# Performance work log

Hardware: AMD Instinct MI355X
Metric: run time of the kernel (lower is better)

## Reference

```python
import math
import jax, jax.numpy as jnp
import numpy as np

B, S, D, H = 2, 2048, 1024, 16


def setup_inputs() -> dict:
    key = jax.random.key(0)
    ks = jax.random.split(key, 8)
    scale = 1.0 / math.sqrt(D)
    kv_mask = jax.random.randint(ks[1], (B, S), 0, 2).astype(bool)
    kv_mask = kv_mask.at[:, 0].set(True)  # ensure at least one valid kv per batch
    return {
        "q": jax.random.normal(ks[0], (B, S, D), dtype=jnp.float32),
        "kv_mask": kv_mask,
        "Wq": jax.random.normal(ks[2], (D, D), dtype=jnp.float32) * scale,
        "Wk": jax.random.normal(ks[3], (D, D), dtype=jnp.float32) * scale,
        "Wv": jax.random.normal(ks[4], (D, D), dtype=jnp.float32) * scale,
        "Wo": jax.random.normal(ks[5], (D, D), dtype=jnp.float32) * scale,
        "bo": jax.random.normal(ks[6], (D,), dtype=jnp.float32) * 0.01,
        "num_heads": H,
    }


def _pass_with_mask(x, W, mask, b=None):
    # Linear applied everywhere, output zeroed where mask is False (pass_with_mask)
    y = x @ W.T
    if b is not None:
        y = y + b
    return jnp.where(mask[..., None], y, 0.0)


def reference(q, kv_mask, Wq, Wk, Wv, Wo, bo, num_heads):
    b, s, d = q.shape
    hd = d // num_heads
    q_mask = jnp.ones((b, s), dtype=bool)  # default q_mask in the module
    # self-attention: k = v = q
    qh = _pass_with_mask(q, Wq, q_mask).reshape(b, s, num_heads, hd)
    kh = _pass_with_mask(q, Wk, kv_mask).reshape(b, s, num_heads, hd)
    vh = _pass_with_mask(q, Wv, kv_mask).reshape(b, s, num_heads, hd)
    # scores: note the module scales by sqrt(model_dim), NOT sqrt(head_dim)
    scores = jnp.einsum("bqhd,bkhd->bhqk", qh, kh) / math.sqrt(d)
    mask = (q_mask[:, :, None] & kv_mask[:, None, :])[:, None, :, :]  # [b,1,q,k]
    scores = jnp.where(mask, scores, -jnp.inf)
    attn = jax.nn.softmax(scores, axis=-1)
    attn = jnp.where(mask, attn, 0.0)
    out = jnp.einsum("bhqk,bkhd->bqhd", attn, vh).reshape(b, s, d)
    return _pass_with_mask(out, Wo, q_mask, bo)
```

## Files before the change

### kernel.cpp

```cpp
#include <hip/hip_runtime.h>
#include <math.h>

#define B_ 2
#define S_ 2048
#define DM 1024
#define NH 16
#define HD 64

typedef unsigned short u16;
typedef unsigned int u32;
typedef __attribute__((ext_vector_type(8))) short bf16x8;
typedef __attribute__((ext_vector_type(4))) float f32x4;

#define C2SCALE 0.0450842200277800f

__device__ __forceinline__ u16 f2bf(float x) {
  unsigned u = __float_as_uint(x);
  u = (u + 0x7FFFu + ((u >> 16) & 1u)) >> 16;
  return (u16)u;
}

__device__ __forceinline__ u32 cvtpk(float lo, float hi) {
  u32 r;
  asm("v_cvt_pk_bf16_f32 %0, %1, %2" : "=v"(r) : "v"(lo), "v"(hi));
  return r;
}

__device__ __forceinline__ float exp2a(float x) {
  float r;
  asm("v_exp_f32 %0, %1" : "=v"(r) : "v"(x));
  return r;
}

__device__ __forceinline__ void gload_lds16(const u16* g, u16* l) {
  __builtin_amdgcn_global_load_lds((const __attribute__((address_space(1))) void*)g,
                                   (__attribute__((address_space(3))) void*)l, 16, 0, 0);
}

__device__ __forceinline__ int sigpos(int w6) {
  return ((w6 >> 5) << 5) | (((w6 >> 2) & 3) << 3) | (((w6 >> 4) & 1) << 2) | (w6 & 3);
}

__global__ void cvt_all(const float* __restrict__ q, const float* __restrict__ Wq,
                        const float* __restrict__ Wk, const float* __restrict__ Wv,
                        const float* __restrict__ Wo, const int* __restrict__ kvm,
                        u16* __restrict__ Xbf, u16* __restrict__ Wcat,
                        u16* __restrict__ Wobf, u16* __restrict__ mwg) {
  const int NQ4 = (B_ * S_ * DM) / 4;
  const int NW4 = (DM * DM) / 4;
  const int total = NQ4 + 4 * NW4;
  int i = blockIdx.x * blockDim.x + threadIdx.x;
  int stride = gridDim.x * blockDim.x;
  for (int t = i; t < B_ * S_; t += stride) {
    int kv = t & (S_ - 1);
    mwg[(t & ~(S_ - 1)) + (kv & ~63) + sigpos(kv & 63)] = kvm[t] ? 0xFFFFu : 0u;
  }
  for (; i < total; i += stride) {
    const float* src;
    u16* dst;
    if (i < NQ4) {
      src = q + (size_t)i * 4; dst = Xbf + (size_t)i * 4;
    } else {
      int t = i - NQ4;
      if (t < NW4)            { src = Wq + (size_t)t * 4; dst = Wcat + (size_t)t * 4; }
      else if (t < 2 * NW4)   { src = Wk + (size_t)(t - NW4) * 4;     dst = Wcat + DM * DM + (size_t)(t - NW4) * 4; }
      else if (t < 3 * NW4)   { src = Wv + (size_t)(t - 2 * NW4) * 4; dst = Wcat + 2 * DM * DM + (size_t)(t - 2 * NW4) * 4; }
      else                    { src = Wo + (size_t)(t - 3 * NW4) * 4; dst = Wobf + (size_t)(t - 3 * NW4) * 4; }
    }
    float4 v = *(const float4*)src;
    ushort4 o;
    o.x = f2bf(v.x); o.y = f2bf(v.y); o.z = f2bf(v.z); o.w = f2bf(v.w);
    *(ushort4*)dst = o;
  }
}

__global__ __launch_bounds__(256, 2) void gemm_bt(
    const u16* __restrict__ A, const u16* __restrict__ Bw, int K,
    u16* __restrict__ qo, u16* __restrict__ ko, u16* __restrict__ vo) {
  __shared__ __align__(16) u16 As[128 * 32];
  __shared__ __align__(16) u16 Bs[128 * 32];
  const int tid = threadIdx.x;
  const int wv = tid >> 6, lane = tid & 63;
  const int g = lane >> 4, c = lane & 15;
  const int wr = wv >> 1, wc = wv & 1;
  const int L = blockIdx.y * gridDim.x + blockIdx.x;
  const int cpx = (gridDim.x * gridDim.y) >> 3;
  const int Ls = (L & 7) * cpx + (L >> 3);
  const int Mb = (Ls & 31) << 7, Nb = (Ls >> 5) << 7;

  f32x4 acc[4][4];
#pragma unroll
  for (int i = 0; i < 4; i++)
#pragma unroll
    for (int j = 0; j < 4; j++) acc[i][j] = f32x4{0.f, 0.f, 0.f, 0.f};

  for (int kb = 0; kb < K; kb += 32) {
#pragma unroll
    for (int it = 0; it < 2; ++it) {
      int id = it * 256 + tid;
      int m = id >> 2, kk = (id & 3) * 8;
      gload_lds16(A + (size_t)(Mb + m) * K + kb + kk, As + (it * 4 + wv) * 512);
      gload_lds16(Bw + (size_t)(Nb + m) * K + kb + kk, Bs + (it * 4 + wv) * 512);
    }
    __syncthreads();
    bf16x8 af[4], bfr[4];
#pragma unroll
    for (int mi = 0; mi < 4; mi++)
      af[mi] = *(const bf16x8*)(As + (wr * 64 + mi * 16 + c) * 32 + g * 8);
#pragma unroll
    for (int ni = 0; ni < 4; ni++)
      bfr[ni] = *(const bf16x8*)(Bs + (wc * 64 + ni * 16 + c) * 32 + g * 8);
#pragma unroll
    for (int mi = 0; mi < 4; mi++)
#pragma unroll
      for (int ni = 0; ni < 4; ni++)
        acc[mi][ni] = __builtin_amdgcn_mfma_f32_16x16x32_bf16(af[mi], bfr[ni], acc[mi][ni], 0, 0, 0);
    __syncthreads();
  }

#pragma unroll
  for (int mi = 0; mi < 4; mi++) {
#pragma unroll
    for (int ni = 0; ni < 4; ni++) {
      int n = Nb + wc * 64 + ni * 16 + c;
      int which = n >> 10, nn = n & 1023;
      int h = nn >> 6, d = nn & 63;
      int row0 = Mb + wr * 64 + mi * 16 + g * 4;
      int b0 = row0 >> 11, s0 = row0 & 2047;
      if (which == 2) {
        int pos = sigpos(s0 & 63);
        uint2 o;
        o.x = cvtpk(acc[mi][ni][0], acc[mi][ni][1]);
        o.y = cvtpk(acc[mi][ni][2], acc[mi][ni][3]);
        *(uint2*)(vo + ((size_t)((b0 * NH + h) * HD + d)) * S_ + (s0 & ~63) + pos) = o;
      } else if (which == 0) {
#pragma unroll
        for (int r = 0; r < 4; r++)
          qo[(((size_t)(b0 * NH + h)) * S_ + s0 + r) * HD + d] =
              f2bf(acc[mi][ni][r] * C2SCALE);
      } else {
#pragma unroll
        for (int r = 0; r < 4; r++)
          ko[(((size_t)(b0 * NH + h)) * S_ + s0 + r) * HD + d] = f2bf(acc[mi][ni][r]);
      }
    }
  }
}

__global__ __launch_bounds__(256, 4) void gemm_n64(
    const u16* __restrict__ A, const u16* __restrict__ Bw,
    const float* __restrict__ bias, float* __restrict__ fo) {
  __shared__ __align__(16) u16 As[128 * 32];
  __shared__ __align__(16) u16 Bs[64 * 32];
  const int K = DM, N = DM;
  const int tid = threadIdx.x;
  const int wv = tid >> 6, lane = tid & 63;
  const int g = lane >> 4, c = lane & 15;
  const int wr = wv >> 1, wc = wv & 1;
  const int L = blockIdx.x;
  const int Ls = (L & 7) * 64 + (L >> 3);
  const int Mb = (Ls & 31) << 7, Nb = (Ls >> 5) << 6;

  f32x4 acc[4][2];
#pragma unroll
  for (int i = 0; i < 4; i++)
#pragma unroll
    for (int j = 0; j < 2; j++) acc[i][j] = f32x4{0.f, 0.f, 0.f, 0.f};

  for (int kb = 0; kb < K; kb += 32) {
#pragma unroll
    for (int it = 0; it < 2; ++it) {
      int id = it * 256 + tid;
      int m = id >> 2, kk = (id & 3) * 8;
      gload_lds16(A + (size_t)(Mb + m) * K + kb + kk, As + (it * 4 + wv) * 512);
    }
    {
      int m = tid >> 2, kk = (tid & 3) * 8;
      gload_lds16(Bw + (size_t)(Nb + m) * K + kb + kk, Bs + wv * 512);
    }
    __syncthreads();
    bf16x8 af[4], bfr[2];
#pragma unroll
    for (int mi = 0; mi < 4; mi++)
      af[mi] = *(const bf16x8*)(As + (wr * 64 + mi * 16 + c) * 32 + g * 8);
#pragma unroll
    for (int ni = 0; ni < 2; ni++)
      bfr[ni] = *(const bf16x8*)(Bs + (wc * 32 + ni * 16 + c) * 32 + g * 8);
#pragma unroll
    for (int mi = 0; mi < 4; mi++)
#pragma unroll
      for (int ni = 0; ni < 2; ni++)
        acc[mi][ni] = __builtin_amdgcn_mfma_f32_16x16x32_bf16(af[mi], bfr[ni], acc[mi][ni], 0, 0, 0);
    __syncthreads();
  }

#pragma unroll
  for (int mi = 0; mi < 4; mi++) {
#pragma unroll
    for (int ni = 0; ni < 2; ni++) {
      int n = Nb + wc * 32 + ni * 16 + c;
      float bv = bias[n];
#pragma unroll
      for (int r = 0; r < 4; r++) {
        int row = Mb + wr * 64 + mi * 16 + g * 4 + r;
        fo[(size_t)row * N + n] = acc[mi][ni][r] + bv;
      }
    }
  }
}

__global__ __launch_bounds__(512, 4) void attn_kernel(
    const u16* __restrict__ qb, const u16* __restrict__ kb,
    const u16* __restrict__ vtb, const u16* __restrict__ mwg,
    u16* __restrict__ ob) {
  __shared__ __align__(16) u16 Kl[2][64 * 64];
  __shared__ __align__(16) u16 Vl[2][64 * 64];
  __shared__ __align__(16) u16 MW[S_];

  const int tid = threadIdx.x;
  const int wv = tid >> 6, lane = tid & 63;
  const int g = lane >> 4, c = lane & 15;

  const int L = blockIdx.x;
  const int j = L >> 3;
  const int bh = ((L & 7) << 2) | (j >> 4);
  const int qi = j & 15;
  const int b = bh >> 4, h = bh & 15;
  const int q0 = qi * 128;
  const size_t bhbase = (size_t)bh * (S_ * HD);

  ((uint2*)MW)[tid] = ((const uint2*)(mwg + b * S_))[tid];

  bf16x8 qf[2];
#pragma unroll
  for (int ks = 0; ks < 2; ks++)
    qf[ks] = *(const bf16x8*)(qb + bhbase + (size_t)(q0 + wv * 16 + c) * HD + ks * 32 + g * 8);

  f32x4 Oa[4];
#pragma unroll
  for (int di = 0; di < 4; di++) Oa[di] = f32x4{0.f, 0.f, 0.f, 0.f};
  f32x4 lacc = f32x4{0.f, 0.f, 0.f, 0.f};

  union { u32 u[4]; bf16x8 v; } ones;
#pragma unroll
  for (int w = 0; w < 4; w++) ones.u[w] = 0x3F803F80u;

  const int srow = tid >> 3;
  const int scol8 = tid & 7;
  const u16* kg = kb + bhbase + (size_t)srow * HD + scol8 * 8;
  const u16* vg = vtb + bhbase + (size_t)srow * S_ + scol8 * 8;
  const int wslot = scol8 ^ (srow & 7);
  u16* kld = &Kl[0][srow * 64 + wslot * 8];
  u16* vld = &Vl[0][srow * 64 + wslot * 8];

  bf16x8 krg = *(const bf16x8*)kg;
  bf16x8 vrg = *(const bf16x8*)vg;
  *(bf16x8*)kld = krg;
  *(bf16x8*)vld = vrg;
  krg = *(const bf16x8*)(kg + 64 * HD);
  vrg = *(const bf16x8*)(vg + 64);
  __syncthreads();

  const int swz = c & 7;
  const int NT = 32;

  for (int t = 0; t < NT; ++t) {
    const int cur = t & 1;
    if (t + 1 < NT) {
      *(bf16x8*)(kld + (cur ^ 1) * 4096) = krg;
      *(bf16x8*)(vld + (cur ^ 1) * 4096) = vrg;
      if (t + 2 < NT) {
        krg = *(const bf16x8*)(kg + (t + 2) * (64 * HD));
        vrg = *(const bf16x8*)(vg + (t + 2) * 64);
      }
    }
    const u16* KB = &Kl[cur][0];
    const u16* VB = &Vl[cur][0];

    f32x4 Sa[4];
#pragma unroll
    for (int ni = 0; ni < 4; ni++) Sa[ni] = f32x4{0.f, 0.f, 0.f, 0.f};
    __builtin_amdgcn_s_setprio(1);
#pragma unroll
    for (int ks = 0; ks < 2; ks++) {
      bf16x8 kf[4];
#pragma unroll
      for (int ni = 0; ni < 4; ni++)
        kf[ni] = *(const bf16x8*)&KB[(ni * 16 + c) * 64 + (((4 * ks + g) ^ swz) * 8)];
#pragma unroll
      for (int ni = 0; ni < 4; ni++)
        Sa[ni] = __builtin_amdgcn_mfma_f32_16x16x32_bf16(kf[ni], qf[ks], Sa[ni], 0, 0, 0);
    }
    __builtin_amdgcn_s_setprio(0);

    bf16x8 Pa[2];
#pragma unroll
    for (int ks = 0; ks < 2; ks++) {
      uint4 mw = *(const uint4*)&MW[t * 64 + ks * 32 + g * 8];
      union { u32 u[4]; bf16x8 v; } pw;
      pw.u[0] = cvtpk(exp2a(Sa[2 * ks][0]), exp2a(Sa[2 * ks][1])) & mw.x;
      pw.u[1] = cvtpk(exp2a(Sa[2 * ks][2]), exp2a(Sa[2 * ks][3])) & mw.y;
      pw.u[2] = cvtpk(exp2a(Sa[2 * ks + 1][0]), exp2a(Sa[2 * ks + 1][1])) & mw.z;
      pw.u[3] = cvtpk(exp2a(Sa[2 * ks + 1][2]), exp2a(Sa[2 * ks + 1][3])) & mw.w;
      Pa[ks] = pw.v;
    }

    __builtin_amdgcn_s_setprio(1);
    lacc = __builtin_amdgcn_mfma_f32_16x16x32_bf16(ones.v, Pa[0], lacc, 0, 0, 0);
    lacc = __builtin_amdgcn_mfma_f32_16x16x32_bf16(ones.v, Pa[1], lacc, 0, 0, 0);
#pragma unroll
    for (int ks = 0; ks < 2; ks++) {
      bf16x8 vf[4];
#pragma unroll
      for (int di = 0; di < 4; di++)
        vf[di] = *(const bf16x8*)&VB[(di * 16 + c) * 64 + (((4 * ks + g) ^ swz) * 8)];
#pragma unroll
      for (int di = 0; di < 4; di++)
        Oa[di] = __builtin_amdgcn_mfma_f32_16x16x32_bf16(vf[di], Pa[ks], Oa[di], 0, 0, 0);
    }
    __builtin_amdgcn_s_setprio(0);

    asm volatile("s_waitcnt lgkmcnt(0)\n\ts_barrier" ::: "memory");
  }

  float inv = 1.f / lacc[0];
  int q = q0 + wv * 16 + c;
  size_t base = ((size_t)(b * S_ + q)) * DM + (size_t)h * HD;
#pragma unroll
  for (int di = 0; di < 4; di++) {
    uint2 o;
    o.x = cvtpk(Oa[di][0] * inv, Oa[di][1] * inv);
    o.y = cvtpk(Oa[di][2] * inv, Oa[di][3] * inv);
    *(uint2*)(ob + base + di * 16 + g * 4) = o;
  }
}

extern "C" void kernel_launch(void* const* d_in, const int* in_sizes, int n_in,
                              void* d_out, int out_size, void* d_ws, size_t ws_size,
                              hipStream_t stream) {
  const float* q  = (const float*)d_in[0];
  const int* kvm  = (const int*)d_in[1];
  const float* Wq = (const float*)d_in[2];
  const float* Wk = (const float*)d_in[3];
  const float* Wv = (const float*)d_in[4];
  const float* Wo = (const float*)d_in[5];
  const float* bo = (const float*)d_in[6];
  float* out = (float*)d_out;
  char* ws = (char*)d_ws;

  u16* Xbf   = (u16*)(ws);
  u16* Wcat  = (u16*)(ws + (8u << 20));
  u16* Wobf  = (u16*)(ws + (14u << 20));
  u16* qbuf  = (u16*)(ws + (16u << 20));
  u16* kbuf  = (u16*)(ws + (24u << 20));
  u16* vtbuf = (u16*)(ws + (32u << 20));
  u16* mwg   = (u16*)(ws + (40u << 20));
  u16* obuf  = Xbf;

  cvt_all<<<2048, 256, 0, stream>>>(q, Wq, Wk, Wv, Wo, kvm, Xbf, Wcat, Wobf, mwg);
  gemm_bt<<<dim3(32, 24), 256, 0, stream>>>(Xbf, Wcat, DM, qbuf, kbuf, vtbuf);
  attn_kernel<<<512, 512, 0, stream>>>(qbuf, kbuf, vtbuf, mwg, obuf);
  gemm_n64<<<512, 256, 0, stream>>>(obuf, Wobf, bo, out);
}
```

Measured before the change: 110.3 us.

## Compact valid KV rows via prefix scan and skip masked attention tiles

A new mask_scan kernel computes prefix positions of valid keys per batch, and the QKV GEMM epilogue writes K and V only for valid rows into compacted positions. The attention kernel then iterates only over ceil(nvalid/64) tiles instead of all 32, and the mask becomes a simple prefix mask. This cuts attention work roughly in proportion to the masked fraction (about half with random masks), at the cost of an extra small launch, scattered row-wise K/V stores in the GEMM epilogue, and padding-zero writes for V.

```diff
diff --git a/kernel.cpp b/kernel.cpp
--- a/kernel.cpp
+++ b/kernel.cpp
@@ -41,19 +41,54 @@
   return ((w6 >> 5) << 5) | (((w6 >> 2) & 3) << 3) | (((w6 >> 4) & 1) << 2) | (w6 & 3);
 }
 
+__global__ void mask_scan(const int* __restrict__ kvm, int* __restrict__ posb,
+                          int* __restrict__ nvb, u16* __restrict__ mwg) {
+  const int b = blockIdx.x;
+  const int tid = threadIdx.x;
+  const int lane = tid & 63, wv = tid >> 6;
+  __shared__ int wsum[4];
+  int v[8], s = 0;
+  const int base = b * S_ + tid * 8;
+#pragma unroll
+  for (int j = 0; j < 8; j++) { v[j] = kvm[base + j] ? 1 : 0; s += v[j]; }
+  int sc = s;
+#pragma unroll
+  for (int off = 1; off < 64; off <<= 1) {
+    int t = __shfl_up(sc, off, 64);
+    if (lane >= off) sc += t;
+  }
+  if (lane == 63) wsum[wv] = sc;
+  __syncthreads();
+  int woff = 0;
+#pragma unroll
+  for (int w = 0; w < 4; w++) woff += (w < wv) ? wsum[w] : 0;
+  int run = woff + sc - s;
+#pragma unroll
+  for (int j = 0; j < 8; j++) { posb[base + j] = run; run += v[j]; }
+  const int total = wsum[0] + wsum[1] + wsum[2] + wsum[3];
+  if (tid == 0) nvb[b] = total;
+  for (int i = tid; i < S_; i += 256)
+    mwg[b * S_ + (i & ~63) + sigpos(i & 63)] = (i < total) ? 0xFFFFu : 0u;
+}
+
 __global__ void cvt_all(const float* __restrict__ q, const float* __restrict__ Wq,
                         const float* __restrict__ Wk, const float* __restrict__ Wv,
-                        const float* __restrict__ Wo, const int* __restrict__ kvm,
+                        const float* __restrict__ Wo, const int* __restrict__ nvb,
                         u16* __restrict__ Xbf, u16* __restrict__ Wcat,
-                        u16* __restrict__ Wobf, u16* __restrict__ mwg) {
+                        u16* __restrict__ Wobf, u16* __restrict__ vtbuf) {
   const int NQ4 = (B_ * S_ * DM) / 4;
   const int NW4 = (DM * DM) / 4;
   const int total = NQ4 + 4 * NW4;
   int i = blockIdx.x * blockDim.x + threadIdx.x;
   int stride = gridDim.x * blockDim.x;
-  for (int t = i; t < B_ * S_; t += stride) {
-    int kv = t & (S_ - 1);
-    mwg[(t & ~(S_ - 1)) + (kv & ~63) + sigpos(kv & 63)] = kvm[t] ? 0xFFFFu : 0u;
+  for (int idx = i; idx < B_ * NH * HD * 64; idx += stride) {
+    int col = idx & 63;
+    int dd = (idx >> 6) & 63;
+    int bh = idx >> 12;
+    int nv = nvb[bh >> 4];
+    int padw = ((nv + 63) & ~63) - nv;
+    if (col < padw)
+      vtbuf[((size_t)bh * HD + dd) * S_ + nv + col] = 0;
   }
   for (; i < total; i += stride) {
     const float* src;
@@ -76,7 +111,8 @@
 
 __global__ __launch_bounds__(256, 2) void gemm_bt(
     const u16* __restrict__ A, const u16* __restrict__ Bw, int K,
-    u16* __restrict__ qo, u16* __restrict__ ko, u16* __restrict__ vo) {
+    u16* __restrict__ qo, u16* __restrict__ ko, u16* __restrict__ vo,
+    const int* __restrict__ kvm, const int* __restrict__ posb) {
   __shared__ __align__(16) u16 As[128 * 32];
   __shared__ __align__(16) u16 Bs[128 * 32];
   const int tid = threadIdx.x;
@@ -118,30 +154,59 @@
     __syncthreads();
   }
 
-#pragma unroll
-  for (int mi = 0; mi < 4; mi++) {
-#pragma unroll
-    for (int ni = 0; ni < 4; ni++) {
-      int n = Nb + wc * 64 + ni * 16 + c;
-      int which = n >> 10, nn = n & 1023;
-      int h = nn >> 6, d = nn & 63;
-      int row0 = Mb + wr * 64 + mi * 16 + g * 4;
-      int b0 = row0 >> 11, s0 = row0 & 2047;
-      if (which == 2) {
-        int pos = sigpos(s0 & 63);
-        uint2 o;
-        o.x = cvtpk(acc[mi][ni][0], acc[mi][ni][1]);
-        o.y = cvtpk(acc[mi][ni][2], acc[mi][ni][3]);
-        *(uint2*)(vo + ((size_t)((b0 * NH + h) * HD + d)) * S_ + (s0 & ~63) + pos) = o;
-      } else if (which == 0) {
-#pragma unroll
-        for (int r = 0; r < 4; r++)
-          qo[(((size_t)(b0 * NH + h)) * S_ + s0 + r) * HD + d] =
+  const int nbase = Nb + wc * 64 + c;
+  const int which = nbase >> 10;
+  if (which == 0) {
+#pragma unroll
+    for (int mi = 0; mi < 4; mi++) {
+#pragma unroll
+      for (int ni = 0; ni < 4; ni++) {
+        int nn = nbase + ni * 16;
+        int h = nn >> 6, d = nn & 63;
+#pragma unroll
+        for (int r = 0; r < 4; r++) {
+          int row = Mb + wr * 64 + mi * 16 + g * 4 + r;
+          int b0 = row >> 11, s0 = row & 2047;
+          qo[(((size_t)(b0 * NH + h)) * S_ + s0) * HD + d] =
               f2bf(acc[mi][ni][r] * C2SCALE);
-      } else {
-#pragma unroll
-        for (int r = 0; r < 4; r++)
-          ko[(((size_t)(b0 * NH + h)) * S_ + s0 + r) * HD + d] = f2bf(acc[mi][ni][r]);
+        }
+      }
+    }
+  } else if (which == 1) {
+#pragma unroll
+    for (int mi = 0; mi < 4; mi++) {
+#pragma unroll
+      for (int r = 0; r < 4; r++) {
+        int row = Mb + wr * 64 + mi * 16 + g * 4 + r;
+        int b0 = row >> 11, s0 = row & 2047;
+        if (kvm[b0 * S_ + s0]) {
+          int p = posb[b0 * S_ + s0];
+#pragma unroll
+          for (int ni = 0; ni < 4; ni++) {
+            int nn = (nbase + ni * 16) & 1023;
+            ko[((size_t)(b0 * NH + (nn >> 6)) * S_ + p) * HD + (nn & 63)] =
+                f2bf(acc[mi][ni][r]);
+          }
+        }
+      }
+    }
+  } else {
+#pragma unroll
+    for (int mi = 0; mi < 4; mi++) {
+#pragma unroll
+      for (int r = 0; r < 4; r++) {
+        int row = Mb + wr * 64 + mi * 16 + g * 4 + r;
+        int b0 = row >> 11, s0 = row & 2047;
+        if (kvm[b0 * S_ + s0]) {
+          int p = posb[b0 * S_ + s0];
+          int dst = (p & ~63) + sigpos(p & 63);
+#pragma unroll
+          for (int ni = 0; ni < 4; ni++) {
+            int nn = (nbase + ni * 16) & 1023;
+            vo[((size_t)((b0 * NH + (nn >> 6)) * HD + (nn & 63))) * S_ + dst] =
+                f2bf(acc[mi][ni][r]);
+          }
+        }
       }
     }
   }
@@ -212,7 +277,7 @@
 __global__ __launch_bounds__(512, 4) void attn_kernel(
     const u16* __restrict__ qb, const u16* __restrict__ kb,
     const u16* __restrict__ vtb, const u16* __restrict__ mwg,
-    u16* __restrict__ ob) {
+    const int* __restrict__ nvb, u16* __restrict__ ob) {
   __shared__ __align__(16) u16 Kl[2][64 * 64];
   __shared__ __align__(16) u16 Vl[2][64 * 64];
   __shared__ __align__(16) u16 MW[S_];
@@ -228,6 +293,7 @@
   const int b = bh >> 4, h = bh & 15;
   const int q0 = qi * 128;
   const size_t bhbase = (size_t)bh * (S_ * HD);
+  const int NT = (nvb[b] + 63) >> 6;
 
   ((uint2*)MW)[tid] = ((const uint2*)(mwg + b * S_))[tid];
 
@@ -262,7 +328,6 @@
   __syncthreads();
 
   const int swz = c & 7;
-  const int NT = 32;
 
   for (int t = 0; t < NT; ++t) {
     const int cur = t & 1;
@@ -355,10 +420,14 @@
   u16* kbuf  = (u16*)(ws + (24u << 20));
   u16* vtbuf = (u16*)(ws + (32u << 20));
   u16* mwg   = (u16*)(ws + (40u << 20));
+  int* posb  = (int*)(ws + (41u << 20));
+  int* nvb   = (int*)(ws + (42u << 20));
   u16* obuf  = Xbf;
 
-  cvt_all<<<2048, 256, 0, stream>>>(q, Wq, Wk, Wv, Wo, kvm, Xbf, Wcat, Wobf, mwg);
-  gemm_bt<<<dim3(32, 24), 256, 0, stream>>>(Xbf, Wcat, DM, qbuf, kbuf, vtbuf);
-  attn_kernel<<<512, 512, 0, stream>>>(qbuf, kbuf, vtbuf, mwg, obuf);
+  mask_scan<<<B_, 256, 0, stream>>>(kvm, posb, nvb, mwg);
+  cvt_all<<<2048, 256, 0, stream>>>(q, Wq, Wk, Wv, Wo, nvb, Xbf, Wcat, Wobf, vtbuf);
+  gemm_bt<<<dim3(32, 24), 256, 0, stream>>>(Xbf, Wcat, DM, qbuf, kbuf, vtbuf,
+                                            kvm, posb);
+  attn_kernel<<<512, 512, 0, stream>>>(qbuf, kbuf, vtbuf, mwg, nvb, obuf);
   gemm_n64<<<512, 256, 0, stream>>>(obuf, Wobf, bo, out);
 }
```

Result: no change. 109.1 us (-1.1%).
